# Kernel tuning notes

Measured on AMD Instinct MI355X. Metric: run time of the kernel, lower is better.

The kernel has to match this reference:

```python
import jax, jax.numpy as jnp
import numpy as np

N_HEADS = 16

def setup_inputs() -> dict:
    key = jax.random.key(0)
    k1, k2, k3 = jax.random.split(key, 3)
    B, S, V = 4, 2048, 1024
    hs = V // N_HEADS
    x = jax.random.normal(k1, (B, S, V), dtype=jnp.float32)
    # per-head shared QKV projection: Linear(head_size, 3*head_size), weight [3*hs, hs]
    W_qkv = jax.random.normal(k2, (3 * hs, hs), dtype=jnp.float32) / np.sqrt(hs)
    W_out = jax.random.normal(k3, (V, V), dtype=jnp.float32) / np.sqrt(V)
    return {"x": x, "W_qkv": W_qkv, "W_out": W_out}

def reference(x, W_qkv, W_out):
    B, S, V = x.shape
    hs = V // N_HEADS
    x_head = x.reshape(B, S, N_HEADS, hs)            # [B,S,H,hs]
    qkv = jnp.einsum('bshd,ed->bshe', x_head, W_qkv)  # [B,S,H,3*hs]
    q, k, v = jnp.split(qkv, 3, axis=-1)
    scale = 1.0 / np.sqrt(hs).astype(np.float32)
    scores = jnp.einsum('bqhd,bkhd->bhqk', q, k) * scale  # [B,H,S,S]
    causal = jnp.tril(jnp.ones((S, S), dtype=bool))       # keep j <= i
    scores = jnp.where(causal, scores, -jnp.inf)
    attn = jax.nn.softmax(scores, axis=-1)                # dropout p=0 (eval)
    o = jnp.einsum('bhqk,bkhd->bqhd', attn, v).reshape(B, S, V)
    return o @ W_out.T
```

## Files before the change

kernel.cpp:

```cpp
#include <hip/hip_runtime.h>

#define B_  4
#define S_  2048
#define V_  1024
#define H_  16
#define HS_ 64
#define GK_ 1024
#define GN_ 1024

typedef unsigned short u16;
typedef __bf16 bf16x8 __attribute__((ext_vector_type(8)));
typedef float  f32x4  __attribute__((ext_vector_type(4)));

__device__ __forceinline__ float bf2f(u16 u) {
  return __uint_as_float(((unsigned int)u) << 16);
}
__device__ __forceinline__ float lo16(unsigned int w) { return __uint_as_float(w << 16); }
__device__ __forceinline__ float hi16(unsigned int w) { return __uint_as_float(w & 0xffff0000u); }
__device__ __forceinline__ u16 f2bf(float f) {
  unsigned int u = __float_as_uint(f);
  unsigned int r = u + 0x7fffu + ((u >> 16) & 1u);
  return (u16)(r >> 16);
}
__device__ __forceinline__ unsigned int cvtpk(float lo, float hi) {
  unsigned int r;
  asm("v_cvt_pk_bf16_f32 %0, %1, %2" : "=v"(r) : "v"(lo), "v"(hi));
  return r;
}

__global__ __launch_bounds__(256) void detect_kernel(
    const unsigned int* __restrict__ x32, int* __restrict__ flag)
{
  __shared__ int zred[256];
  __shared__ int nred[256];
  const int tid = threadIdx.x;
  int nz = 0, nn = 0;
  for (int i = tid; i < 16384; i += 256) {
    unsigned int lo = x32[i] & 0xffffu;
    if (lo == 0u) nz++;
    if ((lo & 0x7f80u) == 0x7f80u && (lo & 0x7fu) != 0u) nn++;
  }
  zred[tid] = nz; nred[tid] = nn;
  __syncthreads();
  for (int s = 128; s > 0; s >>= 1) {
    if (tid < s) { zred[tid] += zred[tid + s]; nred[tid] += nred[tid + s]; }
    __syncthreads();
  }
  if (tid == 0) *flag = (zred[0] > 8192 || nred[0] > 0) ? 1 : 0;
}

__global__ __launch_bounds__(256) void wcvt_kernel(
    const void* __restrict__ w, u16* __restrict__ wb, const int* __restrict__ flag)
{
  const int i = (blockIdx.x * 256 + threadIdx.x) * 4;
  if (*flag) {
    float4 f = *(const float4*)((const float*)w + i);
    unsigned int p0 = (unsigned int)f2bf(f.x) | ((unsigned int)f2bf(f.y) << 16);
    unsigned int p1 = (unsigned int)f2bf(f.z) | ((unsigned int)f2bf(f.w) << 16);
    *(uint2*)(wb + i) = make_uint2(p0, p1);
  } else {
    *(uint2*)(wb + i) = *(const uint2*)((const u16*)w + i);
  }
}

__global__ __launch_bounds__(256) void qkv_mfma_kernel(
    const void* __restrict__ x, const void* __restrict__ wqkv,
    u16* __restrict__ q, u16* __restrict__ k, u16* __restrict__ v,
    const int* __restrict__ flag)
{
  __shared__ __align__(16) u16 Ws[192 * 80];
  const int tid = threadIdx.x;
  const int isf32 = *flag;
  for (int idx = tid; idx < 192 * 4; idx += 256) {
    const int row = idx >> 2, c0 = (idx & 3) * 16;
    u16 t16[16];
    if (isf32) {
      const float4* gp = (const float4*)((const float*)wqkv + row * 64 + c0);
      float4 f0 = gp[0], f1 = gp[1], f2 = gp[2], f3 = gp[3];
      t16[0]=f2bf(f0.x); t16[1]=f2bf(f0.y); t16[2]=f2bf(f0.z); t16[3]=f2bf(f0.w);
      t16[4]=f2bf(f1.x); t16[5]=f2bf(f1.y); t16[6]=f2bf(f1.z); t16[7]=f2bf(f1.w);
      t16[8]=f2bf(f2.x); t16[9]=f2bf(f2.y); t16[10]=f2bf(f2.z); t16[11]=f2bf(f2.w);
      t16[12]=f2bf(f3.x); t16[13]=f2bf(f3.y); t16[14]=f2bf(f3.z); t16[15]=f2bf(f3.w);
    } else {
      const u16* gp = (const u16*)wqkv + row * 64 + c0;
      *(uint4*)t16 = *(const uint4*)gp;
      *(uint4*)(t16 + 8) = *(const uint4*)(gp + 8);
    }
    *(uint4*)(Ws + row * 80 + c0) = *(uint4*)t16;
    *(uint4*)(Ws + row * 80 + c0 + 8) = *(uint4*)(t16 + 8);
  }
  __syncthreads();

  const int m0 = blockIdx.x * 128;
  const int w = tid >> 6, lane = tid & 63;
  const int ar = lane & 15, quad = lane >> 4;
  const int rbase = m0 + (w & 1) * 64;
  const int cbase = (w >> 1) * 96;

  bf16x8 af[4][2];
#pragma unroll
  for (int rt = 0; rt < 4; ++rt) {
    const size_t row = (size_t)(rbase + rt * 16 + ar) * 64;
    if (isf32) {
      const float* gp = (const float*)x + row;
#pragma unroll
      for (int ks = 0; ks < 2; ++ks) {
        const float4* g4 = (const float4*)(gp + ks * 32 + quad * 8);
        float4 f0 = g4[0], f1 = g4[1];
        u16 t8[8];
        t8[0]=f2bf(f0.x); t8[1]=f2bf(f0.y); t8[2]=f2bf(f0.z); t8[3]=f2bf(f0.w);
        t8[4]=f2bf(f1.x); t8[5]=f2bf(f1.y); t8[6]=f2bf(f1.z); t8[7]=f2bf(f1.w);
        af[rt][ks] = *(bf16x8*)t8;
      }
    } else {
      const u16* gp = (const u16*)x + row;
#pragma unroll
      for (int ks = 0; ks < 2; ++ks)
        af[rt][ks] = *(const bf16x8*)(gp + ks * 32 + quad * 8);
    }
  }

  f32x4 acc[4][6] = {};
#pragma unroll
  for (int ks = 0; ks < 2; ++ks)
#pragma unroll
    for (int t = 0; t < 6; ++t) {
      const bf16x8 bfr = *(const bf16x8*)(Ws + (cbase + t * 16 + ar) * 80 + ks * 32 + quad * 8);
#pragma unroll
      for (int rt = 0; rt < 4; ++rt)
        acc[rt][t] = __builtin_amdgcn_mfma_f32_16x16x32_bf16(af[rt][ks], bfr, acc[rt][t], 0, 0, 0);
    }

#pragma unroll
  for (int rt = 0; rt < 4; ++rt)
#pragma unroll
    for (int r = 0; r < 4; ++r) {
      const int m = rbase + rt * 16 + quad * 4 + r;
      const int z = m >> 15, s = (m >> 4) & (S_ - 1), h = m & (H_ - 1);
      const size_t base = (((size_t)z * H_ + h) * S_ + s) * HS_;
#pragma unroll
      for (int t = 0; t < 6; ++t) {
        const int e = cbase + t * 16 + ar;
        u16* dst = (e < 64) ? q : (e < 128) ? k : v;
        dst[base + (e & 63)] = f2bf(acc[rt][t][r]);
      }
    }
}

__global__ __launch_bounds__(256) void qkv_kernel(
    const void* __restrict__ x, int b0, const void* __restrict__ w,
    u16* __restrict__ q, u16* __restrict__ k, u16* __restrict__ v,
    const int* __restrict__ flag)
{
  __shared__ __align__(16) float Ws[192 * 64];
  const int tid = threadIdx.x;
  const int isf32 = *flag;
  if (isf32) {
    for (int i = tid; i < 192 * 64; i += 256) Ws[i] = ((const float*)w)[i];
  } else {
    for (int i = tid; i < 192 * 64; i += 256) Ws[i] = bf2f(((const u16*)w)[i]);
  }
  __syncthreads();

  const int th = blockIdx.x * 256 + tid;
  const int h = th & (H_ - 1);
  const int s = th >> 4;
  const int b = b0 + blockIdx.z;
  const size_t zoff = (size_t)blockIdx.z * H_ * S_ * HS_;
  const size_t xoff = ((size_t)b * S_ + s) * V_ + h * HS_;

  float xf[64];
  if (isf32) {
    const float4* xp = (const float4*)((const float*)x + xoff);
#pragma unroll
    for (int i = 0; i < 16; ++i) {
      float4 u = xp[i];
      xf[4*i+0] = u.x; xf[4*i+1] = u.y; xf[4*i+2] = u.z; xf[4*i+3] = u.w;
    }
  } else {
    const uint4* xp = (const uint4*)((const u16*)x + xoff);
#pragma unroll
    for (int i = 0; i < 8; ++i) {
      uint4 u = xp[i];
      xf[8*i+0] = lo16(u.x); xf[8*i+1] = hi16(u.x);
      xf[8*i+2] = lo16(u.y); xf[8*i+3] = hi16(u.y);
      xf[8*i+4] = lo16(u.z); xf[8*i+5] = hi16(u.z);
      xf[8*i+6] = lo16(u.w); xf[8*i+7] = hi16(u.w);
    }
  }

  const size_t obase = zoff + ((size_t)h * S_ + s) * HS_;
#pragma unroll 1
  for (int eg = 0; eg < 12; ++eg) {
    float acc[16];
#pragma unroll
    for (int ee = 0; ee < 16; ++ee) {
      const float4* wr = (const float4*)&Ws[(eg * 16 + ee) * 64];
      float a = 0.f;
#pragma unroll
      for (int d4 = 0; d4 < 16; ++d4) {
        float4 wv = wr[d4];
        a += xf[d4*4+0]*wv.x + xf[d4*4+1]*wv.y + xf[d4*4+2]*wv.z + xf[d4*4+3]*wv.w;
      }
      acc[ee] = a;
    }
    u16* dst = (eg < 4) ? q : (eg < 8) ? k : v;
    const int d0 = (eg & 3) * 16;
    unsigned int p[8];
#pragma unroll
    for (int t = 0; t < 8; ++t)
      p[t] = (unsigned int)f2bf(acc[2*t]) | ((unsigned int)f2bf(acc[2*t+1]) << 16);
    uint4* dp = (uint4*)(dst + obase + d0);
    dp[0] = make_uint4(p[0], p[1], p[2], p[3]);
    dp[1] = make_uint4(p[4], p[5], p[6], p[7]);
  }
}

__global__ __launch_bounds__(256, 4) void attn_mfma_kernel(
    const u16* __restrict__ q, const u16* __restrict__ k,
    const u16* __restrict__ v, u16* __restrict__ o)
{
  const int z   = blockIdx.z;
  const int h   = blockIdx.y;
  const int bi  = blockIdx.x;
  const int qb0 = bi * 64;
  const int qb1 = (31 - bi) * 64;
  const int tid = threadIdx.x;
  const int w = tid >> 6, lane = tid & 63;
  const int col = lane & 15, quad = lane >> 4;

  __shared__ __align__(16) u16 Ks[64 * 72];
  __shared__ __align__(16) u16 Vt[64 * 72];
  __shared__ __align__(16) u16 Ps[4][16 * 72];

  const size_t hs = ((size_t)z * H_ + h) * S_ * HS_;

  const float qs = 0.125f * 1.44269504089f;
  bf16x8 qf[2][2];
#pragma unroll
  for (int u = 0; u < 2; ++u) {
    const int qb = u ? qb1 : qb0;
    const u16* qp = q + hs + (size_t)(qb + w * 16 + col) * HS_ + quad * 8;
#pragma unroll
    for (int ks = 0; ks < 2; ++ks) {
      u16 t8[8];
      *(uint4*)t8 = *(const uint4*)(qp + ks * 32);
#pragma unroll
      for (int e = 0; e < 8; ++e) t8[e] = f2bf(bf2f(t8[e]) * qs);
      qf[u][ks] = *(bf16x8*)t8;
    }
  }

  const int sr = tid >> 2, sc = (tid & 3) * 16;
  const int vr = (tid & 31) * 2, vc = (tid >> 5) * 8;

  f32x4 oacc[2][4] = {};
  float l_run[2] = {0.f, 0.f};

  const int jbmax = qb1;

  uint4 k0, k1, va, vb;
  {
    const u16* kp = k + hs + (size_t)sr * HS_ + sc;
    k0 = *(const uint4*)kp;
    k1 = *(const uint4*)(kp + 8);
    const u16* vp = v + hs + (size_t)vr * HS_ + vc;
    va = *(const uint4*)vp;
    vb = *(const uint4*)(vp + HS_);
  }

  for (int jb = 0; jb <= jbmax; jb += 64) {
    __syncthreads();
    *(uint4*)(Ks + sr * 72 + sc)     = k0;
    *(uint4*)(Ks + sr * 72 + sc + 8) = k1;
    {
      const u16* pa = (const u16*)&va;
      const u16* pb = (const u16*)&vb;
#pragma unroll
      for (int e = 0; e < 8; ++e)
        *(unsigned int*)(Vt + (vc + e) * 72 + vr) =
            (unsigned int)pa[e] | ((unsigned int)pb[e] << 16);
    }
    __syncthreads();

    if (jb < jbmax) {
      const u16* kp = k + hs + (size_t)(jb + 64 + sr) * HS_ + sc;
      k0 = *(const uint4*)kp;
      k1 = *(const uint4*)(kp + 8);
      const u16* vp = v + hs + (size_t)(jb + 64 + vr) * HS_ + vc;
      va = *(const uint4*)vp;
      vb = *(const uint4*)(vp + HS_);
    }

#pragma unroll
    for (int u = 0; u < 2; ++u) {
      const int ru = (u ? qb1 : qb0) + w * 16;
      if (jb > ru + 15) continue;

      f32x4 sacc[4] = {};
      __builtin_amdgcn_s_setprio(1);
#pragma unroll
      for (int ks = 0; ks < 2; ++ks)
#pragma unroll
        for (int t = 0; t < 4; ++t) {
          const bf16x8 kf = *(const bf16x8*)(Ks + (t * 16 + col) * 72 + ks * 32 + quad * 8);
          sacc[t] = __builtin_amdgcn_mfma_f32_16x16x32_bf16(kf, qf[u][ks], sacc[t], 0, 0, 0);
        }
      __builtin_amdgcn_s_setprio(0);

      if (jb + 63 > ru) {
        const int q_l = ru + col;
#pragma unroll
        for (int t = 0; t < 4; ++t) {
          const int kb = jb + t * 16 + quad * 4;
#pragma unroll
          for (int r = 0; r < 4; ++r)
            if (kb + r > q_l) sacc[t][r] = -INFINITY;
        }
      }

      float ls = 0.f;
#pragma unroll
      for (int t = 0; t < 4; ++t) {
        const float p0 = __builtin_amdgcn_exp2f(sacc[t][0]);
        const float p1 = __builtin_amdgcn_exp2f(sacc[t][1]);
        const float p2 = __builtin_amdgcn_exp2f(sacc[t][2]);
        const float p3 = __builtin_amdgcn_exp2f(sacc[t][3]);
        ls += (p0 + p1) + (p2 + p3);
        *(uint2*)(Ps[w] + col * 72 + t * 16 + quad * 4) =
            make_uint2(cvtpk(p0, p1), cvtpk(p2, p3));
      }
      l_run[u] += ls;

      __builtin_amdgcn_s_setprio(1);
#pragma unroll
      for (int ks = 0; ks < 2; ++ks) {
        const bf16x8 pf = *(const bf16x8*)(Ps[w] + col * 72 + ks * 32 + quad * 8);
#pragma unroll
        for (int nt = 0; nt < 4; ++nt) {
          const bf16x8 vf = *(const bf16x8*)(Vt + (nt * 16 + col) * 72 + ks * 32 + quad * 8);
          oacc[u][nt] = __builtin_amdgcn_mfma_f32_16x16x32_bf16(pf, vf, oacc[u][nt], 0, 0, 0);
        }
      }
      __builtin_amdgcn_s_setprio(0);
    }
  }

  u16* ob = o + (size_t)z * S_ * V_ + h * HS_;
#pragma unroll
  for (int u = 0; u < 2; ++u) {
    const int ru = (u ? qb1 : qb0) + w * 16;
    float lt = l_run[u];
    lt += __shfl_xor(lt, 16);
    lt += __shfl_xor(lt, 32);
    float inv[4];
#pragma unroll
    for (int r = 0; r < 4; ++r) inv[r] = 1.0f / __shfl(lt, quad * 4 + r);
#pragma unroll
    for (int nt = 0; nt < 4; ++nt)
#pragma unroll
      for (int r = 0; r < 4; ++r)
        ob[(size_t)(ru + quad * 4 + r) * V_ + nt * 16 + col] = f2bf(oacc[u][nt][r] * inv[r]);
  }
}

__global__ __launch_bounds__(256) void oproj_mfma_kernel(
    const u16* __restrict__ a, const u16* __restrict__ bw, float* __restrict__ c)
{
  __shared__ __align__(16) u16 As[128 * 40];
  __shared__ __align__(16) u16 Bs[128 * 40];
  const int tid = threadIdx.x;
  const int m0 = blockIdx.x * 128;
  const int n0 = blockIdx.y * 128;
  const int w = tid >> 6, lane = tid & 63;
  const int col = lane & 15, quad = lane >> 4;
  const int qr = (w & 1) * 64;
  const int qc = (w >> 1) * 64;

  f32x4 acc[4][4] = {};

  const int sr = tid >> 2;
  const int sk = (tid & 3) * 8;
  const u16* ga = a  + (size_t)(m0 + sr) * GK_ + sk;
  const u16* gb = bw + (size_t)(n0 + sr) * GK_ + sk;

  uint4 a0 = *(const uint4*)(ga);
  uint4 a1 = *(const uint4*)(ga + (size_t)64 * GK_);
  uint4 b0 = *(const uint4*)(gb);
  uint4 b1 = *(const uint4*)(gb + (size_t)64 * GK_);

  for (int k0 = 0; k0 < GK_; k0 += 32) {
    __syncthreads();
    *(uint4*)(As + sr * 40 + sk)        = a0;
    *(uint4*)(As + (64 + sr) * 40 + sk) = a1;
    *(uint4*)(Bs + sr * 40 + sk)        = b0;
    *(uint4*)(Bs + (64 + sr) * 40 + sk) = b1;
    __syncthreads();

    if (k0 + 32 < GK_) {
      a0 = *(const uint4*)(ga + k0 + 32);
      a1 = *(const uint4*)(ga + (size_t)64 * GK_ + k0 + 32);
      b0 = *(const uint4*)(gb + k0 + 32);
      b1 = *(const uint4*)(gb + (size_t)64 * GK_ + k0 + 32);
    }

    bf16x8 af[4], bfr[4];
#pragma unroll
    for (int i = 0; i < 4; ++i) {
      af[i]  = *(const bf16x8*)(As + (qr + i * 16 + col) * 40 + quad * 8);
      bfr[i] = *(const bf16x8*)(Bs + (qc + i * 16 + col) * 40 + quad * 8);
    }
    __builtin_amdgcn_s_setprio(1);
#pragma unroll
    for (int i = 0; i < 4; ++i)
#pragma unroll
      for (int j = 0; j < 4; ++j)
        acc[i][j] = __builtin_amdgcn_mfma_f32_16x16x32_bf16(af[i], bfr[j], acc[i][j], 0, 0, 0);
    __builtin_amdgcn_s_setprio(0);
  }

#pragma unroll
  for (int i = 0; i < 4; ++i)
#pragma unroll
    for (int j = 0; j < 4; ++j)
#pragma unroll
      for (int r = 0; r < 4; ++r)
        c[(size_t)(m0 + qr + i * 16 + quad * 4 + r) * GN_ + n0 + qc + j * 16 + col]
            = acc[i][j][r];
}

__global__ __launch_bounds__(256) void oproj_vec_kernel(
    const u16* __restrict__ o, const void* __restrict__ w,
    float* __restrict__ out, const int* __restrict__ flag)
{
  __shared__ __align__(16) float At[64 * 68];
  __shared__ __align__(16) float Wt[64 * 68];
  const int tid = threadIdx.x;
  const size_t zo = (size_t)blockIdx.z * S_ * V_;
  const int m0 = blockIdx.x * 64;
  const int n0 = blockIdx.y * 64;
  const int tr = tid >> 4, tc = tid & 15;
  const int isf32 = *flag;
  const int srow = tid >> 2, sc = (tid & 3) * 16;

  float acc[4][4] = {};

  for (int k0 = 0; k0 < GK_; k0 += 64) {
    float av[16], wv[16];
    {
      const u16* gp = o + zo + (size_t)(m0 + srow) * GK_ + k0 + sc;
      uint4 u0 = *(const uint4*)gp;
      uint4 u1 = *(const uint4*)(gp + 8);
      av[0]=lo16(u0.x); av[1]=hi16(u0.x); av[2]=lo16(u0.y); av[3]=hi16(u0.y);
      av[4]=lo16(u0.z); av[5]=hi16(u0.z); av[6]=lo16(u0.w); av[7]=hi16(u0.w);
      av[8]=lo16(u1.x); av[9]=hi16(u1.x); av[10]=lo16(u1.y); av[11]=hi16(u1.y);
      av[12]=lo16(u1.z); av[13]=hi16(u1.z); av[14]=lo16(u1.w); av[15]=hi16(u1.w);
    }
    if (isf32) {
      const float4* gp = (const float4*)((const float*)w + (size_t)(n0 + srow) * GK_ + k0 + sc);
#pragma unroll
      for (int i = 0; i < 4; ++i) {
        float4 f = gp[i];
        wv[4*i+0]=f.x; wv[4*i+1]=f.y; wv[4*i+2]=f.z; wv[4*i+3]=f.w;
      }
    } else {
      const u16* gp = (const u16*)w + (size_t)(n0 + srow) * GK_ + k0 + sc;
      uint4 u0 = *(const uint4*)gp;
      uint4 u1 = *(const uint4*)(gp + 8);
      wv[0]=lo16(u0.x); wv[1]=hi16(u0.x); wv[2]=lo16(u0.y); wv[3]=hi16(u0.y);
      wv[4]=lo16(u0.z); wv[5]=hi16(u0.z); wv[6]=lo16(u0.w); wv[7]=hi16(u0.w);
      wv[8]=lo16(u1.x); wv[9]=hi16(u1.x); wv[10]=lo16(u1.y); wv[11]=hi16(u1.y);
      wv[12]=lo16(u1.z); wv[13]=hi16(u1.z); wv[14]=lo16(u1.w); wv[15]=hi16(u1.w);
    }
    __syncthreads();
#pragma unroll
    for (int i = 0; i < 16; ++i) {
      At[(sc + i) * 68 + srow] = av[i];
      Wt[(sc + i) * 68 + srow] = wv[i];
    }
    __syncthreads();

#pragma unroll 4
    for (int kk = 0; kk < 64; ++kk) {
      float4 a4 = *(const float4*)&At[kk * 68 + tr * 4];
      float4 w4 = *(const float4*)&Wt[kk * 68 + tc * 4];
      acc[0][0] += a4.x*w4.x; acc[0][1] += a4.x*w4.y; acc[0][2] += a4.x*w4.z; acc[0][3] += a4.x*w4.w;
      acc[1][0] += a4.y*w4.x; acc[1][1] += a4.y*w4.y; acc[1][2] += a4.y*w4.z; acc[1][3] += a4.y*w4.w;
      acc[2][0] += a4.z*w4.x; acc[2][1] += a4.z*w4.y; acc[2][2] += a4.z*w4.z; acc[2][3] += a4.z*w4.w;
      acc[3][0] += a4.w*w4.x; acc[3][1] += a4.w*w4.y; acc[3][2] += a4.w*w4.z; acc[3][3] += a4.w*w4.w;
    }
  }

#pragma unroll
  for (int r = 0; r < 4; ++r) {
    const int row = m0 + tr * 4 + r;
    *(float4*)(out + zo + (size_t)row * GN_ + n0 + tc * 4) =
        make_float4(acc[r][0], acc[r][1], acc[r][2], acc[r][3]);
  }
}

extern "C" void kernel_launch(void* const* d_in, const int* in_sizes, int n_in,
                              void* d_out, int out_size, void* d_ws, size_t ws_size,
                              hipStream_t stream) {
  const void* x = d_in[0];
  const void* wqkv = (n_in > 1) ? d_in[1] : d_in[0];
  const void* wout = (n_in > 2) ? d_in[2] : d_in[0];
  for (int i = 0; i < n_in; ++i) {
    if      (in_sizes[i] == B_ * S_ * V_)  x    = d_in[i];
    else if (in_sizes[i] == 3 * HS_ * HS_) wqkv = d_in[i];
    else if (in_sizes[i] == V_ * V_)       wout = d_in[i];
  }
  float* out = (float*)d_out;

  const size_t per_b = (size_t)H_ * S_ * HS_;
  const size_t SV = (size_t)S_ * V_;
  int* flag = (int*)d_ws;
  const bool full = ws_size >= (16 + 16 * per_b * sizeof(u16));
  const size_t stride = full ? 4 * per_b : per_b;
  u16* q = (u16*)((char*)d_ws + 16);
  u16* k = q + stride;
  u16* v = k + stride;
  u16* o = v + stride;

  detect_kernel<<<dim3(1), dim3(256), 0, stream>>>((const unsigned int*)x, flag);
  if (full) {
    qkv_mfma_kernel<<<dim3((B_ * S_ * H_) / 128), dim3(256), 0, stream>>>(
        x, wqkv, q, k, v, flag);
    attn_mfma_kernel<<<dim3(16, 16, B_), dim3(256), 0, stream>>>(q, k, v, o);
    u16* wb = q;
    wcvt_kernel<<<dim3((V_ * V_) / 1024), dim3(256), 0, stream>>>(wout, wb, flag);
    oproj_mfma_kernel<<<dim3((B_ * S_) / 128, GN_ / 128), dim3(256), 0, stream>>>(o, wb, out);
  } else {
    for (int b = 0; b < B_; ++b) {
      qkv_kernel<<<dim3(128, 1, 1), dim3(256), 0, stream>>>(x, b, wqkv, q, k, v, flag);
      attn_mfma_kernel<<<dim3(16, 16, 1), dim3(256), 0, stream>>>(q, k, v, o);
      oproj_vec_kernel<<<dim3(32, 16, 1), dim3(256), 0, stream>>>(
          o, wout, out + (size_t)b * SV, flag);
    }
  }
}
```

Measured before the change: 215.5 us.

## Split paired causal query blocks into separate blocks, heaviest first

The attention kernel previously gave each block two 64-row query tiles (one early, one late), so every block did the same amount of causal work and shared its K/V tile loads between them. Now each block handles a single query tile, the grid doubles to 32 blocks per head, and blocks are issued from the longest causal range down. This gives more blocks for the scheduler to spread across CUs and lowers register use per thread. In exchange each K/V tile is loaded once per query tile instead of once per pair, and load balance now depends on the hardware scheduler.

```diff
diff --git a/kernel.cpp b/kernel.cpp
--- a/kernel.cpp
+++ b/kernel.cpp
@@ -222,12 +222,11 @@
 {
   const int z   = blockIdx.z;
   const int h   = blockIdx.y;
-  const int bi  = blockIdx.x;
-  const int qb0 = bi * 64;
-  const int qb1 = (31 - bi) * 64;
+  const int qb  = (31 - blockIdx.x) * 64;
   const int tid = threadIdx.x;
   const int w = tid >> 6, lane = tid & 63;
   const int col = lane & 15, quad = lane >> 4;
+  const int ru = qb + w * 16;
 
   __shared__ __align__(16) u16 Ks[64 * 72];
   __shared__ __align__(16) u16 Vt[64 * 72];
@@ -236,28 +235,24 @@
   const size_t hs = ((size_t)z * H_ + h) * S_ * HS_;
 
   const float qs = 0.125f * 1.44269504089f;
-  bf16x8 qf[2][2];
-#pragma unroll
-  for (int u = 0; u < 2; ++u) {
-    const int qb = u ? qb1 : qb0;
-    const u16* qp = q + hs + (size_t)(qb + w * 16 + col) * HS_ + quad * 8;
+  bf16x8 qf[2];
+  {
+    const u16* qp = q + hs + (size_t)(ru + col) * HS_ + quad * 8;
 #pragma unroll
     for (int ks = 0; ks < 2; ++ks) {
       u16 t8[8];
       *(uint4*)t8 = *(const uint4*)(qp + ks * 32);
 #pragma unroll
       for (int e = 0; e < 8; ++e) t8[e] = f2bf(bf2f(t8[e]) * qs);
-      qf[u][ks] = *(bf16x8*)t8;
+      qf[ks] = *(bf16x8*)t8;
     }
   }
 
   const int sr = tid >> 2, sc = (tid & 3) * 16;
   const int vr = (tid & 31) * 2, vc = (tid >> 5) * 8;
 
-  f32x4 oacc[2][4] = {};
-  float l_run[2] = {0.f, 0.f};
-
-  const int jbmax = qb1;
+  f32x4 oacc[4] = {};
+  float l_run = 0.f;
 
   uint4 k0, k1, va, vb;
   {
@@ -269,7 +264,7 @@
     vb = *(const uint4*)(vp + HS_);
   }
 
-  for (int jb = 0; jb <= jbmax; jb += 64) {
+  for (int jb = 0; jb <= qb; jb += 64) {
     __syncthreads();
     *(uint4*)(Ks + sr * 72 + sc)     = k0;
     *(uint4*)(Ks + sr * 72 + sc + 8) = k1;
@@ -283,7 +278,7 @@
     }
     __syncthreads();
 
-    if (jb < jbmax) {
+    if (jb < qb) {
       const u16* kp = k + hs + (size_t)(jb + 64 + sr) * HS_ + sc;
       k0 = *(const uint4*)kp;
       k1 = *(const uint4*)(kp + 8);
@@ -292,76 +287,66 @@
       vb = *(const uint4*)(vp + HS_);
     }
 
-#pragma unroll
-    for (int u = 0; u < 2; ++u) {
-      const int ru = (u ? qb1 : qb0) + w * 16;
-      if (jb > ru + 15) continue;
-
-      f32x4 sacc[4] = {};
-      __builtin_amdgcn_s_setprio(1);
-#pragma unroll
-      for (int ks = 0; ks < 2; ++ks)
-#pragma unroll
-        for (int t = 0; t < 4; ++t) {
-          const bf16x8 kf = *(const bf16x8*)(Ks + (t * 16 + col) * 72 + ks * 32 + quad * 8);
-          sacc[t] = __builtin_amdgcn_mfma_f32_16x16x32_bf16(kf, qf[u][ks], sacc[t], 0, 0, 0);
-        }
-      __builtin_amdgcn_s_setprio(0);
-
-      if (jb + 63 > ru) {
-        const int q_l = ru + col;
-#pragma unroll
-        for (int t = 0; t < 4; ++t) {
-          const int kb = jb + t * 16 + quad * 4;
-#pragma unroll
-          for (int r = 0; r < 4; ++r)
-            if (kb + r > q_l) sacc[t][r] = -INFINITY;
-        }
-      }
-
-      float ls = 0.f;
+    f32x4 sacc[4] = {};
+    __builtin_amdgcn_s_setprio(1);
+#pragma unroll
+    for (int ks = 0; ks < 2; ++ks)
 #pragma unroll
       for (int t = 0; t < 4; ++t) {
-        const float p0 = __builtin_amdgcn_exp2f(sacc[t][0]);
-        const float p1 = __builtin_amdgcn_exp2f(sacc[t][1]);
-        const float p2 = __builtin_amdgcn_exp2f(sacc[t][2]);
-        const float p3 = __builtin_amdgcn_exp2f(sacc[t][3]);
-        ls += (p0 + p1) + (p2 + p3);
-        *(uint2*)(Ps[w] + col * 72 + t * 16 + quad * 4) =
-            make_uint2(cvtpk(p0, p1), cvtpk(p2, p3));
-      }
-      l_run[u] += ls;
-
-      __builtin_amdgcn_s_setprio(1);
-#pragma unroll
-      for (int ks = 0; ks < 2; ++ks) {
-        const bf16x8 pf = *(const bf16x8*)(Ps[w] + col * 72 + ks * 32 + quad * 8);
-#pragma unroll
-        for (int nt = 0; nt < 4; ++nt) {
-          const bf16x8 vf = *(const bf16x8*)(Vt + (nt * 16 + col) * 72 + ks * 32 + quad * 8);
-          oacc[u][nt] = __builtin_amdgcn_mfma_f32_16x16x32_bf16(pf, vf, oacc[u][nt], 0, 0, 0);
-        }
-      }
-      __builtin_amdgcn_s_setprio(0);
-    }
+        const bf16x8 kf = *(const bf16x8*)(Ks + (t * 16 + col) * 72 + ks * 32 + quad * 8);
+        sacc[t] = __builtin_amdgcn_mfma_f32_16x16x32_bf16(kf, qf[ks], sacc[t], 0, 0, 0);
+      }
+    __builtin_amdgcn_s_setprio(0);
+
+    if (jb == qb) {
+      const int q_l = ru + col;
+#pragma unroll
+      for (int t = 0; t < 4; ++t) {
+        const int kb = jb + t * 16 + quad * 4;
+#pragma unroll
+        for (int r = 0; r < 4; ++r)
+          if (kb + r > q_l) sacc[t][r] = -INFINITY;
+      }
+    }
+
+    float ls = 0.f;
+#pragma unroll
+    for (int t = 0; t < 4; ++t) {
+      const float p0 = __builtin_amdgcn_exp2f(sacc[t][0]);
+      const float p1 = __builtin_amdgcn_exp2f(sacc[t][1]);
+      const float p2 = __builtin_amdgcn_exp2f(sacc[t][2]);
+      const float p3 = __builtin_amdgcn_exp2f(sacc[t][3]);
+      ls += (p0 + p1) + (p2 + p3);
+      *(uint2*)(Ps[w] + col * 72 + t * 16 + quad * 4) =
+          make_uint2(cvtpk(p0, p1), cvtpk(p2, p3));
+    }
+    l_run += ls;
+
+    __builtin_amdgcn_s_setprio(1);
+#pragma unroll
+    for (int ks = 0; ks < 2; ++ks) {
+      const bf16x8 pf = *(const bf16x8*)(Ps[w] + col * 72 + ks * 32 + quad * 8);
+#pragma unroll
+      for (int nt = 0; nt < 4; ++nt) {
+        const bf16x8 vf = *(const bf16x8*)(Vt + (nt * 16 + col) * 72 + ks * 32 + quad * 8);
+        oacc[nt] = __builtin_amdgcn_mfma_f32_16x16x32_bf16(pf, vf, oacc[nt], 0, 0, 0);
+      }
+    }
+    __builtin_amdgcn_s_setprio(0);
   }
 
   u16* ob = o + (size_t)z * S_ * V_ + h * HS_;
-#pragma unroll
-  for (int u = 0; u < 2; ++u) {
-    const int ru = (u ? qb1 : qb0) + w * 16;
-    float lt = l_run[u];
-    lt += __shfl_xor(lt, 16);
-    lt += __shfl_xor(lt, 32);
-    float inv[4];
-#pragma unroll
-    for (int r = 0; r < 4; ++r) inv[r] = 1.0f / __shfl(lt, quad * 4 + r);
-#pragma unroll
-    for (int nt = 0; nt < 4; ++nt)
-#pragma unroll
-      for (int r = 0; r < 4; ++r)
-        ob[(size_t)(ru + quad * 4 + r) * V_ + nt * 16 + col] = f2bf(oacc[u][nt][r] * inv[r]);
-  }
+  float lt = l_run;
+  lt += __shfl_xor(lt, 16);
+  lt += __shfl_xor(lt, 32);
+  float inv[4];
+#pragma unroll
+  for (int r = 0; r < 4; ++r) inv[r] = 1.0f / __shfl(lt, quad * 4 + r);
+#pragma unroll
+  for (int nt = 0; nt < 4; ++nt)
+#pragma unroll
+    for (int r = 0; r < 4; ++r)
+      ob[(size_t)(ru + quad * 4 + r) * V_ + nt * 16 + col] = f2bf(oacc[nt][r] * inv[r]);
 }
 
 __global__ __launch_bounds__(256) void oproj_mfma_kernel(
@@ -526,14 +511,14 @@
   if (full) {
     qkv_mfma_kernel<<<dim3((B_ * S_ * H_) / 128), dim3(256), 0, stream>>>(
         x, wqkv, q, k, v, flag);
-    attn_mfma_kernel<<<dim3(16, 16, B_), dim3(256), 0, stream>>>(q, k, v, o);
+    attn_mfma_kernel<<<dim3(32, 16, B_), dim3(256), 0, stream>>>(q, k, v, o);
     u16* wb = q;
     wcvt_kernel<<<dim3((V_ * V_) / 1024), dim3(256), 0, stream>>>(wout, wb, flag);
     oproj_mfma_kernel<<<dim3((B_ * S_) / 128, GN_ / 128), dim3(256), 0, stream>>>(o, wb, out);
   } else {
     for (int b = 0; b < B_; ++b) {
       qkv_kernel<<<dim3(128, 1, 1), dim3(256), 0, stream>>>(x, b, wqkv, q, k, v, flag);
-      attn_mfma_kernel<<<dim3(16, 16, 1), dim3(256), 0, stream>>>(q, k, v, o);
+      attn_mfma_kernel<<<dim3(32, 16, 1), dim3(256), 0, stream>>>(q, k, v, o);
       oproj_vec_kernel<<<dim3(32, 16, 1), dim3(256), 0, stream>>>(
           o, wout, out + (size_t)b * SV, flag);
     }
```

Measured after the change: 267.1 us. +23.9%, slower.
